# Kernel optimization log

Measured on AMD Instinct MI355X. Metric: run time of the kernel, lower is better.

## Reference

```python
import jax, jax.numpy as jnp
import numpy as np

DIM = 1024
NUM_HEADS = 16
HEAD_DIM = DIM // NUM_HEADS
SCALE = HEAD_DIM ** -0.5


def setup_inputs() -> dict:
    key = jax.random.key(0)
    k1, k2, k3 = jax.random.split(key, 3)
    B, N = 2, 2048
    x = jax.random.normal(k1, (B, N, DIM), dtype=jnp.float32)
    # qkv: Linear(dim, 3*dim, bias=False); proj: Linear(dim, dim) with bias
    w_qkv = jax.random.normal(k2, (3 * DIM, DIM), dtype=jnp.float32) * (DIM ** -0.5)
    w_proj = jax.random.normal(k3, (DIM, DIM), dtype=jnp.float32) * (DIM ** -0.5)
    b_proj = jnp.zeros((DIM,), dtype=jnp.float32)
    return {"x": x, "w_qkv": w_qkv, "w_proj": w_proj, "b_proj": b_proj}


def reference(x, w_qkv, w_proj, b_proj):
    B, N, C = x.shape
    H, D = NUM_HEADS, HEAD_DIM
    qkv = jnp.einsum('bnc,fc->bnf', x, w_qkv)                 # [B,N,3C]
    qkv = qkv.reshape(B, N, 3, H, D).transpose(2, 0, 3, 1, 4)  # [3,B,H,N,D]
    q, k, v = qkv[0], qkv[1], qkv[2]
    q = q * SCALE
    attn = jnp.einsum('bhnd,bhmd->bhnm', q, k)                 # [B,H,N,N]
    attn = jax.nn.softmax(attn, axis=-1)
    out = jnp.einsum('bhnm,bhmd->bhnd', attn, v)               # [B,H,N,D]
    out = out.transpose(0, 2, 1, 3).reshape(B, N, C)
    out = jnp.einsum('bnc,fc->bnf', out, w_proj) + b_proj
    return out
```

## Files before the change

### kernel.cpp

```cpp
#include <hip/hip_runtime.h>
#include <hip/hip_bf16.h>
#include <stdint.h>

typedef __attribute__((ext_vector_type(4))) float f32x4;
typedef __attribute__((ext_vector_type(16))) float f32x16;
typedef __attribute__((ext_vector_type(8))) short bf16x8;
typedef __attribute__((ext_vector_type(4))) short bf16x4;
typedef unsigned short ushort_t;

#define QSCALE 0.18033688f

__device__ inline short f2bf(float f) {
  unsigned u = __builtin_bit_cast(unsigned, f);
  u += 0x7fffu + ((u >> 16) & 1u);
  return (short)(u >> 16);
}

__device__ inline void gload_lds16(const void* g, void* l) {
  __builtin_amdgcn_global_load_lds(
      (const __attribute__((address_space(1))) void*)g,
      (__attribute__((address_space(3))) void*)l, 16, 0, 0);
}

__device__ inline unsigned cvtpk(float a, float b) {
  unsigned r;
  asm("v_cvt_pk_bf16_f32 %0, %1, %2" : "=v"(r) : "v"(a), "v"(b));
  return r;
}

__device__ inline void swap32u(unsigned& a, unsigned& b) {
  asm("v_permlane32_swap_b32 %0, %1" : "+v"(a), "+v"(b));
}

__global__ __launch_bounds__(256) void cvt_all(const float* __restrict__ x,
                                               const float* __restrict__ wq,
                                               const float* __restrict__ wp,
                                               short* __restrict__ Xb,
                                               short* __restrict__ Wq,
                                               short* __restrict__ Wp) {
  int i = blockIdx.x * 256 + threadIdx.x;
  const float* s;
  short* d;
  int off;
  if (i < 524288)       { s = x;  d = Xb; off = i; }
  else if (i < 917504)  { s = wq; d = Wq; off = i - 524288; }
  else                  { s = wp; d = Wp; off = i - 917504; }
  const float4* sv = (const float4*)s;
  float4 a = sv[2 * off], b = sv[2 * off + 1];
  bf16x8 o;
  o[0] = f2bf(a.x); o[1] = f2bf(a.y); o[2] = f2bf(a.z); o[3] = f2bf(a.w);
  o[4] = f2bf(b.x); o[5] = f2bf(b.y); o[6] = f2bf(b.z); o[7] = f2bf(b.w);
  ((bf16x8*)d)[off] = o;
}

template <int BN, int F32OUT>
__global__ __launch_bounds__(256, 3) void gemm_pipe(const short* __restrict__ A,
                                                    const short* __restrict__ B,
                                                    void* __restrict__ Cv,
                                                    const float* __restrict__ bias,
                                                    int scale_cols, float scale_val,
                                                    int M, int N, int K) {
  constexpr int MFR = (BN == 128) ? 4 : 2;
  __shared__ short Abuf[3][128 * 32];
  __shared__ short Bbuf[3][BN * 32];
  const int tid = threadIdx.x, wv = tid >> 6, ln = tid & 63;
  const int wm = (BN == 128) ? (wv >> 1) : wv;
  const int wn = (BN == 128) ? (wv & 1) : 0;
  const int bn0 = blockIdx.x * BN, bm0 = blockIdx.y * 128;
  const int nt = K >> 5;

  const int srow = ln >> 2;
  const int scol = (((ln & 3) ^ (srow & 3)) * 8);
  const int fln = ln & 15;
  const int fk = ln >> 4;

  f32x4 acc[MFR][4] = {};

  auto stage = [&](int t, int s) {
    const size_t k0 = (size_t)(t << 5);
#pragma unroll
    for (int rd = 0; rd < 2; rd++) {
      int ch = 2 * wv + rd;
      gload_lds16(A + (size_t)(bm0 + ch * 16 + srow) * K + k0 + scol,
                  (char*)Abuf[s] + ch * 1024);
    }
    if constexpr (BN == 128) {
#pragma unroll
      for (int rd = 0; rd < 2; rd++) {
        int ch = 2 * wv + rd;
        gload_lds16(B + (size_t)(bn0 + ch * 16 + srow) * K + k0 + scol,
                    (char*)Bbuf[s] + ch * 1024);
      }
    } else {
      gload_lds16(B + (size_t)(bn0 + wv * 16 + srow) * K + k0 + scol,
                  (char*)Bbuf[s] + wv * 1024);
    }
  };

  stage(0, 0);
  stage(1, 1);
  if constexpr (BN == 128) asm volatile("s_waitcnt vmcnt(4)" ::: "memory");
  else                     asm volatile("s_waitcnt vmcnt(3)" ::: "memory");
  __builtin_amdgcn_s_barrier();
  __builtin_amdgcn_sched_barrier(0);

  for (int t = 0; t < nt; t++) {
    const int s = t % 3;
    const bool more = (t + 2) < nt;
    if (more) stage(t + 2, (t + 2) % 3);

    const char* Ab = (const char*)Abuf[s];
    const char* Bb = (const char*)Bbuf[s];
    bf16x8 af[MFR], bfr[4];
#pragma unroll
    for (int m = 0; m < MFR; m++) {
      int R = wm * (MFR * 16) + m * 16 + fln;
      af[m] = *(const bf16x8*)(Ab + R * 64 + ((fk ^ (R & 3)) << 4));
    }
#pragma unroll
    for (int n = 0; n < 4; n++) {
      int R = wn * 64 + n * 16 + fln;
      bfr[n] = *(const bf16x8*)(Bb + R * 64 + ((fk ^ (R & 3)) << 4));
    }

    __builtin_amdgcn_s_setprio(1);
#pragma unroll
    for (int m = 0; m < MFR; m++)
#pragma unroll
      for (int n = 0; n < 4; n++)
        acc[m][n] = __builtin_amdgcn_mfma_f32_16x16x32_bf16(af[m], bfr[n], acc[m][n], 0, 0, 0);
    __builtin_amdgcn_s_setprio(0);

    if (more) {
      if constexpr (BN == 128) asm volatile("s_waitcnt vmcnt(4)" ::: "memory");
      else                     asm volatile("s_waitcnt vmcnt(3)" ::: "memory");
    } else {
      asm volatile("s_waitcnt vmcnt(0)" ::: "memory");
    }
    __builtin_amdgcn_s_barrier();
    __builtin_amdgcn_sched_barrier(0);
  }

  const int r0 = bm0 + wm * (MFR * 16), c0 = bn0 + wn * 64;
  const int fg4 = (ln >> 4) * 4;
#pragma unroll
  for (int m = 0; m < MFR; m++)
#pragma unroll
    for (int n = 0; n < 4; n++)
#pragma unroll
      for (int j = 0; j < 4; j++) {
        int row = r0 + m * 16 + fg4 + j;
        int col = c0 + n * 16 + fln;
        float v = acc[m][n][j];
        if (col < scale_cols) v *= scale_val;
        if (F32OUT) ((float*)Cv)[(size_t)row * N + col] = v + bias[col];
        else        ((short*)Cv)[(size_t)row * N + col] = f2bf(v);
      }
}

__global__ __launch_bounds__(256, 2) void attn_fwd(const short* __restrict__ QKV,
                                                   short* __restrict__ AO) {
  __shared__ short Ks[2][64 * 64];
  __shared__ short Vt[2][64 * 64];
  const int tid = threadIdx.x, wv = tid >> 6, ln = tid & 63;
  const int lq = ln & 31, hi = ln >> 5;
  const int id = blockIdx.x;
  const int c = (id & 7) * 64 + (id >> 3);
  const int qt = c & 15, bh = c >> 4;
  const int b = bh >> 4, h = bh & 15;
  const short* base = QKV + (size_t)b * 2048 * 3072 + h * 64;
  const short* Kg = base + 1024;
  const short* Vg = base + 2048;
  const int qrow = qt * 128 + wv * 32 + lq;

  bf16x8 qf[4];
  {
    const short* Qrow = base + (size_t)qrow * 3072;
#pragma unroll
    for (int ds = 0; ds < 4; ds++)
      qf[ds] = *(const bf16x8*)(Qrow + ds * 16 + hi * 8);
  }

  const int krow = ln >> 3;
  const int kcol = ((ln & 7) ^ (ln >> 3)) * 8;
  const int vrow_b = ln * 128;
  const int vxor = ln & 7;

  float l_run = 0.f;
  f32x16 o0 = {}, o1 = {};
  ushort_t vu[16];

#pragma unroll
  for (int rd = 0; rd < 2; rd++)
    gload_lds16(Kg + (size_t)(16 * wv + 8 * rd + krow) * 3072 + kcol,
                (char*)Ks[0] + (2 * wv + rd) * 1024);
#pragma unroll
  for (int i = 0; i < 16; i++)
    vu[i] = *(const ushort_t*)(Vg + (size_t)(16 * wv + i) * 3072 + ln);
  {
    bf16x8 w0, w1;
#pragma unroll
    for (int i = 0; i < 8; i++) { w0[i] = (short)vu[i]; w1[i] = (short)vu[8 + i]; }
    *(bf16x8*)((char*)Vt[0] + vrow_b + (((2 * wv) ^ vxor) << 4)) = w0;
    *(bf16x8*)((char*)Vt[0] + vrow_b + (((2 * wv + 1) ^ vxor) << 4)) = w1;
  }
  __syncthreads();

  for (int t = 0; t < 32; t++) {
    const int s = t & 1;
    if (t < 31) {
#pragma unroll
      for (int rd = 0; rd < 2; rd++)
        gload_lds16(Kg + (size_t)((t + 1) * 64 + 16 * wv + 8 * rd + krow) * 3072 + kcol,
                    (char*)Ks[s ^ 1] + (2 * wv + rd) * 1024);
#pragma unroll
      for (int i = 0; i < 16; i++)
        vu[i] = *(const ushort_t*)(Vg + (size_t)((t + 1) * 64 + 16 * wv + i) * 3072 + ln);
    }

    f32x16 c0 = {}, c1 = {};
    const char* Kb = (const char*)Ks[s];
    __builtin_amdgcn_s_setprio(1);
#pragma unroll
    for (int ds = 0; ds < 4; ds++) {
      const int cp = (ds * 2 + hi) ^ (lq & 7);
      bf16x8 ka0 = *(const bf16x8*)(Kb + lq * 128 + cp * 16);
      bf16x8 ka1 = *(const bf16x8*)(Kb + (32 + lq) * 128 + cp * 16);
      c0 = __builtin_amdgcn_mfma_f32_32x32x16_bf16(ka0, qf[ds], c0, 0, 0, 0);
      c1 = __builtin_amdgcn_mfma_f32_32x32x16_bf16(ka1, qf[ds], c1, 0, 0, 0);
    }
    __builtin_amdgcn_s_setprio(0);

#pragma unroll
    for (int r = 0; r < 16; r++) c0[r] = __builtin_amdgcn_exp2f(c0[r]);
#pragma unroll
    for (int r = 0; r < 16; r++) c1[r] = __builtin_amdgcn_exp2f(c1[r]);
    {
      float st[8];
#pragma unroll
      for (int r = 0; r < 8; r++)
        st[r] = (c0[2 * r] + c0[2 * r + 1]) + (c1[2 * r] + c1[2 * r + 1]);
#pragma unroll
      for (int r = 0; r < 4; r++) st[r] += st[r + 4];
      l_run += (st[0] + st[1]) + (st[2] + st[3]);
    }

    bf16x8 pa[4];
#pragma unroll
    for (int cs = 0; cs < 2; cs++) {
      const f32x16& p = cs ? c1 : c0;
#pragma unroll
      for (int ksl = 0; ksl < 2; ksl++) {
        unsigned A0 = cvtpk(p[8 * ksl + 0], p[8 * ksl + 1]);
        unsigned A1 = cvtpk(p[8 * ksl + 2], p[8 * ksl + 3]);
        unsigned B0 = cvtpk(p[8 * ksl + 4], p[8 * ksl + 5]);
        unsigned B1 = cvtpk(p[8 * ksl + 6], p[8 * ksl + 7]);
        swap32u(A0, B0);
        swap32u(A1, B1);
        union { unsigned u[4]; bf16x8 v; } tmp;
        tmp.u[0] = A0; tmp.u[1] = A1; tmp.u[2] = B0; tmp.u[3] = B1;
        pa[cs * 2 + ksl] = tmp.v;
      }
    }

    const char* Vb = (const char*)Vt[s];
    __builtin_amdgcn_s_setprio(1);
#pragma unroll
    for (int ks = 0; ks < 4; ks++) {
      const int cp = (ks * 2 + hi) ^ (lq & 7);
      bf16x8 va0 = *(const bf16x8*)(Vb + lq * 128 + cp * 16);
      bf16x8 va1 = *(const bf16x8*)(Vb + (32 + lq) * 128 + cp * 16);
      o0 = __builtin_amdgcn_mfma_f32_32x32x16_bf16(va0, pa[ks], o0, 0, 0, 0);
      o1 = __builtin_amdgcn_mfma_f32_32x32x16_bf16(va1, pa[ks], o1, 0, 0, 0);
    }
    __builtin_amdgcn_s_setprio(0);

    if (t < 31) {
      bf16x8 w0, w1;
#pragma unroll
      for (int i = 0; i < 8; i++) { w0[i] = (short)vu[i]; w1[i] = (short)vu[8 + i]; }
      *(bf16x8*)((char*)Vt[s ^ 1] + vrow_b + (((2 * wv) ^ vxor) << 4)) = w0;
      *(bf16x8*)((char*)Vt[s ^ 1] + vrow_b + (((2 * wv + 1) ^ vxor) << 4)) = w1;
    }
    __syncthreads();
  }

  l_run += __shfl_xor(l_run, 32);
  const float inv = __builtin_amdgcn_rcpf(l_run);
  short* Arow = AO + ((size_t)(b * 2048) + qrow) * 1024 + h * 64;
#pragma unroll
  for (int dt = 0; dt < 2; dt++) {
    const f32x16& o = dt ? o1 : o0;
#pragma unroll
    for (int g = 0; g < 4; g++) {
      bf16x4 w;
#pragma unroll
      for (int i = 0; i < 4; i++) w[i] = f2bf(o[4 * g + i] * inv);
      *(bf16x4*)(Arow + dt * 32 + 8 * g + 4 * hi) = w;
    }
  }
}

extern "C" void kernel_launch(void* const* d_in, const int* in_sizes, int n_in,
                              void* d_out, int out_size, void* d_ws, size_t ws_size,
                              hipStream_t stream) {
  const float* x = (const float*)d_in[0];
  const float* w_qkv = (const float*)d_in[1];
  const float* w_proj = (const float*)d_in[2];
  const float* b_proj = (const float*)d_in[3];
  float* out = (float*)d_out;

  char* ws = (char*)d_ws;
  short* Xb = (short*)(ws + 0);
  short* Wq = (short*)(ws + 8388608);
  short* Wp = (short*)(ws + 14680064);
  short* QKV = (short*)(ws + 16777216);
  short* AO = (short*)(ws + 41943040);

  cvt_all<<<4096, 256, 0, stream>>>(x, w_qkv, w_proj, Xb, Wq, Wp);

  gemm_pipe<128, 0><<<dim3(24, 32), 256, 0, stream>>>(Xb, Wq, QKV, nullptr,
                                                      1024, QSCALE, 4096, 3072, 1024);

  attn_fwd<<<dim3(512), 256, 0, stream>>>(QKV, AO);

  gemm_pipe<64, 1><<<dim3(16, 32), 256, 0, stream>>>(AO, Wp, out, b_proj,
                                                     0, 1.0f, 4096, 1024, 1024);
}
```

Before: 120.4 us.

## Double attention KV tile to 128 keys with split accumulators and earlier V store

```diff
diff --git a/kernel.cpp b/kernel.cpp
--- a/kernel.cpp
+++ b/kernel.cpp
@@ -160,8 +160,8 @@
 
 __global__ __launch_bounds__(256, 2) void attn_fwd(const short* __restrict__ QKV,
                                                    short* __restrict__ AO) {
-  __shared__ short Ks[2][64 * 64];
-  __shared__ short Vt[2][64 * 64];
+  __shared__ short Ks[2][128 * 64];
+  __shared__ short Vt[2][64 * 128];
   const int tid = threadIdx.x, wv = tid >> 6, ln = tid & 63;
   const int lq = ln & 31, hi = ln >> 5;
   const int id = blockIdx.x;
@@ -183,83 +183,116 @@
 
   const int krow = ln >> 3;
   const int kcol = ((ln & 7) ^ (ln >> 3)) * 8;
-  const int vrow_b = ln * 128;
-  const int vxor = ln & 7;
+  const int vrow_b = ln * 256;
+  const int vx = ln & 15;
 
   float l_run = 0.f;
-  f32x16 o0 = {}, o1 = {};
-  ushort_t vu[16];
-
-#pragma unroll
-  for (int rd = 0; rd < 2; rd++)
-    gload_lds16(Kg + (size_t)(16 * wv + 8 * rd + krow) * 3072 + kcol,
-                (char*)Ks[0] + (2 * wv + rd) * 1024);
-#pragma unroll
-  for (int i = 0; i < 16; i++)
-    vu[i] = *(const ushort_t*)(Vg + (size_t)(16 * wv + i) * 3072 + ln);
-  {
-    bf16x8 w0, w1;
-#pragma unroll
-    for (int i = 0; i < 8; i++) { w0[i] = (short)vu[i]; w1[i] = (short)vu[8 + i]; }
-    *(bf16x8*)((char*)Vt[0] + vrow_b + (((2 * wv) ^ vxor) << 4)) = w0;
-    *(bf16x8*)((char*)Vt[0] + vrow_b + (((2 * wv + 1) ^ vxor) << 4)) = w1;
-  }
+  f32x16 oA0 = {}, oA1 = {}, oB0 = {}, oB1 = {};
+  ushort_t vu[32];
+
+#define STAGE_K(ph, s)                                                           \
+  {                                                                              \
+    _Pragma("unroll")                                                            \
+    for (int rd = 0; rd < 4; rd++)                                               \
+      gload_lds16(Kg + (size_t)((ph) * 128 + 32 * wv + 8 * rd + krow) * 3072 + kcol, \
+                  (char*)Ks[s] + (4 * wv + rd) * 1024);                          \
+  }
+#define LOAD_V(ph)                                                               \
+  {                                                                              \
+    _Pragma("unroll")                                                            \
+    for (int i = 0; i < 32; i++)                                                 \
+      vu[i] = *(const ushort_t*)(Vg + (size_t)((ph) * 128 + 32 * wv + i) * 3072 + ln); \
+  }
+#define WRITE_V(s)                                                               \
+  {                                                                              \
+    _Pragma("unroll")                                                            \
+    for (int i = 0; i < 4; i++) {                                                \
+      bf16x8 w;                                                                  \
+      _Pragma("unroll")                                                          \
+      for (int j = 0; j < 8; j++) w[j] = (short)vu[8 * i + j];                   \
+      *(bf16x8*)((char*)Vt[s] + vrow_b + (((4 * wv + i) ^ vx) << 4)) = w;        \
+    }                                                                            \
+  }
+
+  STAGE_K(0, 0);
+  LOAD_V(0);
+  WRITE_V(0);
   __syncthreads();
 
-  for (int t = 0; t < 32; t++) {
+  for (int t = 0; t < 16; t++) {
     const int s = t & 1;
-    if (t < 31) {
-#pragma unroll
-      for (int rd = 0; rd < 2; rd++)
-        gload_lds16(Kg + (size_t)((t + 1) * 64 + 16 * wv + 8 * rd + krow) * 3072 + kcol,
-                    (char*)Ks[s ^ 1] + (2 * wv + rd) * 1024);
-#pragma unroll
-      for (int i = 0; i < 16; i++)
-        vu[i] = *(const ushort_t*)(Vg + (size_t)((t + 1) * 64 + 16 * wv + i) * 3072 + ln);
-    }
-
-    f32x16 c0 = {}, c1 = {};
+    if (t < 15) {
+      STAGE_K(t + 1, s ^ 1);
+      LOAD_V(t + 1);
+    }
+
+    f32x16 cA0 = {}, cA1 = {}, cB0 = {}, cB1 = {};
     const char* Kb = (const char*)Ks[s];
     __builtin_amdgcn_s_setprio(1);
 #pragma unroll
     for (int ds = 0; ds < 4; ds++) {
-      const int cp = (ds * 2 + hi) ^ (lq & 7);
-      bf16x8 ka0 = *(const bf16x8*)(Kb + lq * 128 + cp * 16);
-      bf16x8 ka1 = *(const bf16x8*)(Kb + (32 + lq) * 128 + cp * 16);
-      c0 = __builtin_amdgcn_mfma_f32_32x32x16_bf16(ka0, qf[ds], c0, 0, 0, 0);
-      c1 = __builtin_amdgcn_mfma_f32_32x32x16_bf16(ka1, qf[ds], c1, 0, 0, 0);
+      const int cp = ((ds * 2 + hi) ^ (lq & 7)) << 4;
+      bf16x8 kA0 = *(const bf16x8*)(Kb + lq * 128 + cp);
+      bf16x8 kA1 = *(const bf16x8*)(Kb + (32 + lq) * 128 + cp);
+      bf16x8 kB0 = *(const bf16x8*)(Kb + (64 + lq) * 128 + cp);
+      bf16x8 kB1 = *(const bf16x8*)(Kb + (96 + lq) * 128 + cp);
+      cA0 = __builtin_amdgcn_mfma_f32_32x32x16_bf16(kA0, qf[ds], cA0, 0, 0, 0);
+      cB0 = __builtin_amdgcn_mfma_f32_32x32x16_bf16(kB0, qf[ds], cB0, 0, 0, 0);
+      cA1 = __builtin_amdgcn_mfma_f32_32x32x16_bf16(kA1, qf[ds], cA1, 0, 0, 0);
+      cB1 = __builtin_amdgcn_mfma_f32_32x32x16_bf16(kB1, qf[ds], cB1, 0, 0, 0);
     }
     __builtin_amdgcn_s_setprio(0);
 
-#pragma unroll
-    for (int r = 0; r < 16; r++) c0[r] = __builtin_amdgcn_exp2f(c0[r]);
-#pragma unroll
-    for (int r = 0; r < 16; r++) c1[r] = __builtin_amdgcn_exp2f(c1[r]);
+    if (t < 15) WRITE_V(s ^ 1);
+
+#pragma unroll
+    for (int r = 0; r < 16; r++) cA0[r] = __builtin_amdgcn_exp2f(cA0[r]);
+#pragma unroll
+    for (int r = 0; r < 16; r++) cA1[r] = __builtin_amdgcn_exp2f(cA1[r]);
+#pragma unroll
+    for (int r = 0; r < 16; r++) cB0[r] = __builtin_amdgcn_exp2f(cB0[r]);
+#pragma unroll
+    for (int r = 0; r < 16; r++) cB1[r] = __builtin_amdgcn_exp2f(cB1[r]);
     {
       float st[8];
 #pragma unroll
       for (int r = 0; r < 8; r++)
-        st[r] = (c0[2 * r] + c0[2 * r + 1]) + (c1[2 * r] + c1[2 * r + 1]);
+        st[r] = ((cA0[2 * r] + cA0[2 * r + 1]) + (cA1[2 * r] + cA1[2 * r + 1])) +
+                ((cB0[2 * r] + cB0[2 * r + 1]) + (cB1[2 * r] + cB1[2 * r + 1]));
 #pragma unroll
       for (int r = 0; r < 4; r++) st[r] += st[r + 4];
       l_run += (st[0] + st[1]) + (st[2] + st[3]);
     }
 
-    bf16x8 pa[4];
+    bf16x8 paA[4], paB[4];
 #pragma unroll
     for (int cs = 0; cs < 2; cs++) {
-      const f32x16& p = cs ? c1 : c0;
+      const f32x16& pA = cs ? cA1 : cA0;
+      const f32x16& pB = cs ? cB1 : cB0;
 #pragma unroll
       for (int ksl = 0; ksl < 2; ksl++) {
-        unsigned A0 = cvtpk(p[8 * ksl + 0], p[8 * ksl + 1]);
-        unsigned A1 = cvtpk(p[8 * ksl + 2], p[8 * ksl + 3]);
-        unsigned B0 = cvtpk(p[8 * ksl + 4], p[8 * ksl + 5]);
-        unsigned B1 = cvtpk(p[8 * ksl + 6], p[8 * ksl + 7]);
-        swap32u(A0, B0);
-        swap32u(A1, B1);
-        union { unsigned u[4]; bf16x8 v; } tmp;
-        tmp.u[0] = A0; tmp.u[1] = A1; tmp.u[2] = B0; tmp.u[3] = B1;
-        pa[cs * 2 + ksl] = tmp.v;
+        {
+          unsigned A0 = cvtpk(pA[8 * ksl + 0], pA[8 * ksl + 1]);
+          unsigned A1 = cvtpk(pA[8 * ksl + 2], pA[8 * ksl + 3]);
+          unsigned B0 = cvtpk(pA[8 * ksl + 4], pA[8 * ksl + 5]);
+          unsigned B1 = cvtpk(pA[8 * ksl + 6], pA[8 * ksl + 7]);
+          swap32u(A0, B0);
+          swap32u(A1, B1);
+          union { unsigned u[4]; bf16x8 v; } tmp;
+          tmp.u[0] = A0; tmp.u[1] = A1; tmp.u[2] = B0; tmp.u[3] = B1;
+          paA[cs * 2 + ksl] = tmp.v;
+        }
+        {
+          unsigned A0 = cvtpk(pB[8 * ksl + 0], pB[8 * ksl + 1]);
+          unsigned A1 = cvtpk(pB[8 * ksl + 2], pB[8 * ksl + 3]);
+          unsigned B0 = cvtpk(pB[8 * ksl + 4], pB[8 * ksl + 5]);
+          unsigned B1 = cvtpk(pB[8 * ksl + 6], pB[8 * ksl + 7]);
+          swap32u(A0, B0);
+          swap32u(A1, B1);
+          union { unsigned u[4]; bf16x8 v; } tmp;
+          tmp.u[0] = A0; tmp.u[1] = A1; tmp.u[2] = B0; tmp.u[3] = B1;
+          paB[cs * 2 + ksl] = tmp.v;
+        }
       }
     }
 
@@ -267,35 +300,37 @@
     __builtin_amdgcn_s_setprio(1);
 #pragma unroll
     for (int ks = 0; ks < 4; ks++) {
-      const int cp = (ks * 2 + hi) ^ (lq & 7);
-      bf16x8 va0 = *(const bf16x8*)(Vb + lq * 128 + cp * 16);
-      bf16x8 va1 = *(const bf16x8*)(Vb + (32 + lq) * 128 + cp * 16);
-      o0 = __builtin_amdgcn_mfma_f32_32x32x16_bf16(va0, pa[ks], o0, 0, 0, 0);
-      o1 = __builtin_amdgcn_mfma_f32_32x32x16_bf16(va1, pa[ks], o1, 0, 0, 0);
+      const int cpa = (((ks * 2 + hi) ^ (lq & 15)) << 4);
+      const int cpb = (((8 + ks * 2 + hi) ^ (lq & 15)) << 4);
+      bf16x8 vA0 = *(const bf16x8*)(Vb + lq * 256 + cpa);
+      bf16x8 vA1 = *(const bf16x8*)(Vb + (32 + lq) * 256 + cpa);
+      bf16x8 vB0 = *(const bf16x8*)(Vb + lq * 256 + cpb);
+      bf16x8 vB1 = *(const bf16x8*)(Vb + (32 + lq) * 256 + cpb);
+      oA0 = __builtin_amdgcn_mfma_f32_32x32x16_bf16(vA0, paA[ks], oA0, 0, 0, 0);
+      oB0 = __builtin_amdgcn_mfma_f32_32x32x16_bf16(vB0, paB[ks], oB0, 0, 0, 0);
+      oA1 = __builtin_amdgcn_mfma_f32_32x32x16_bf16(vA1, paA[ks], oA1, 0, 0, 0);
+      oB1 = __builtin_amdgcn_mfma_f32_32x32x16_bf16(vB1, paB[ks], oB1, 0, 0, 0);
     }
     __builtin_amdgcn_s_setprio(0);
 
-    if (t < 31) {
-      bf16x8 w0, w1;
-#pragma unroll
-      for (int i = 0; i < 8; i++) { w0[i] = (short)vu[i]; w1[i] = (short)vu[8 + i]; }
-      *(bf16x8*)((char*)Vt[s ^ 1] + vrow_b + (((2 * wv) ^ vxor) << 4)) = w0;
-      *(bf16x8*)((char*)Vt[s ^ 1] + vrow_b + (((2 * wv + 1) ^ vxor) << 4)) = w1;
-    }
     __syncthreads();
   }
+#undef STAGE_K
+#undef LOAD_V
+#undef WRITE_V
 
   l_run += __shfl_xor(l_run, 32);
   const float inv = __builtin_amdgcn_rcpf(l_run);
   short* Arow = AO + ((size_t)(b * 2048) + qrow) * 1024 + h * 64;
 #pragma unroll
   for (int dt = 0; dt < 2; dt++) {
-    const f32x16& o = dt ? o1 : o0;
+    const f32x16& oa = dt ? oA1 : oA0;
+    const f32x16& ob = dt ? oB1 : oB0;
 #pragma unroll
     for (int g = 0; g < 4; g++) {
       bf16x4 w;
 #pragma unroll
-      for (int i = 0; i < 4; i++) w[i] = f2bf(o[4 * g + i] * inv);
+      for (int i = 0; i < 4; i++) w[i] = f2bf((oa[4 * g + i] + ob[4 * g + i]) * inv);
       *(bf16x4*)(Arow + dt * 32 + 8 * g + 4 * hi) = w;
     }
   }
```

Result: faster. 117.7 us (-2.2%).

## Split attention KV range in two with a separate merge kernel

Applied to the files above, without the earlier changes.

```diff
diff --git a/kernel.cpp b/kernel.cpp
--- a/kernel.cpp
+++ b/kernel.cpp
@@ -14,6 +14,10 @@
   unsigned u = __builtin_bit_cast(unsigned, f);
   u += 0x7fffu + ((u >> 16) & 1u);
   return (short)(u >> 16);
+}
+
+__device__ inline float bf2f(short s) {
+  return __builtin_bit_cast(float, ((unsigned)(ushort_t)s) << 16);
 }
 
 __device__ inline void gload_lds16(const void* g, void* l) {
@@ -158,19 +162,20 @@
       }
 }
 
-__global__ __launch_bounds__(256, 2) void attn_fwd(const short* __restrict__ QKV,
-                                                   short* __restrict__ AO) {
+__global__ __launch_bounds__(256, 4) void attn_fwd(const short* __restrict__ QKV,
+                                                   short* __restrict__ OP,
+                                                   float* __restrict__ Lp) {
   __shared__ short Ks[2][64 * 64];
   __shared__ short Vt[2][64 * 64];
   const int tid = threadIdx.x, wv = tid >> 6, ln = tid & 63;
   const int lq = ln & 31, hi = ln >> 5;
   const int id = blockIdx.x;
-  const int c = (id & 7) * 64 + (id >> 3);
-  const int qt = c & 15, bh = c >> 4;
+  const int c = (id & 7) * 128 + (id >> 3);
+  const int kvs = c & 1, qt = (c >> 1) & 15, bh = c >> 5;
   const int b = bh >> 4, h = bh & 15;
   const short* base = QKV + (size_t)b * 2048 * 3072 + h * 64;
-  const short* Kg = base + 1024;
-  const short* Vg = base + 2048;
+  const short* Kg = base + 1024 + (size_t)(kvs << 10) * 3072;
+  const short* Vg = base + 2048 + (size_t)(kvs << 10) * 3072;
   const int qrow = qt * 128 + wv * 32 + lq;
 
   bf16x8 qf[4];
@@ -206,9 +211,9 @@
   }
   __syncthreads();
 
-  for (int t = 0; t < 32; t++) {
+  for (int t = 0; t < 16; t++) {
     const int s = t & 1;
-    if (t < 31) {
+    if (t < 15) {
 #pragma unroll
       for (int rd = 0; rd < 2; rd++)
         gload_lds16(Kg + (size_t)((t + 1) * 64 + 16 * wv + 8 * rd + krow) * 3072 + kcol,
@@ -275,7 +280,7 @@
     }
     __builtin_amdgcn_s_setprio(0);
 
-    if (t < 31) {
+    if (t < 15) {
       bf16x8 w0, w1;
 #pragma unroll
       for (int i = 0; i < 8; i++) { w0[i] = (short)vu[i]; w1[i] = (short)vu[8 + i]; }
@@ -286,8 +291,9 @@
   }
 
   l_run += __shfl_xor(l_run, 32);
-  const float inv = __builtin_amdgcn_rcpf(l_run);
-  short* Arow = AO + ((size_t)(b * 2048) + qrow) * 1024 + h * 64;
+  const int qcol = wv * 32 + lq;
+  if (hi == 0) Lp[c * 128 + qcol] = l_run;
+  short* Op = OP + (size_t)c * 8192 + qcol * 64;
 #pragma unroll
   for (int dt = 0; dt < 2; dt++) {
     const f32x16& o = dt ? o1 : o0;
@@ -295,9 +301,35 @@
     for (int g = 0; g < 4; g++) {
       bf16x4 w;
 #pragma unroll
-      for (int i = 0; i < 4; i++) w[i] = f2bf(o[4 * g + i] * inv);
-      *(bf16x4*)(Arow + dt * 32 + 8 * g + 4 * hi) = w;
-    }
+      for (int i = 0; i < 4; i++) w[i] = f2bf(o[4 * g + i]);
+      *(bf16x4*)(Op + dt * 32 + 8 * g + 4 * hi) = w;
+    }
+  }
+}
+
+__global__ __launch_bounds__(256) void attn_merge(const short* __restrict__ OP,
+                                                  const float* __restrict__ Lp,
+                                                  short* __restrict__ AO) {
+  const int m = blockIdx.x;
+  const int bh = m >> 4, qt = m & 15;
+  const int b = bh >> 4, h = bh & 15;
+  const int tid = threadIdx.x;
+  const int q = tid & 127, dh = tid >> 7;
+  const int c0 = bh * 32 + qt * 2, c1 = c0 + 1;
+  const float l = Lp[c0 * 128 + q] + Lp[c1 * 128 + q];
+  const float inv = __builtin_amdgcn_rcpf(l);
+  const short* p0 = OP + (size_t)c0 * 8192 + q * 64 + dh * 32;
+  const short* p1 = OP + (size_t)c1 * 8192 + q * 64 + dh * 32;
+  short* dst = AO + ((size_t)(b * 2048 + qt * 128 + q)) * 1024 + h * 64 + dh * 32;
+#pragma unroll
+  for (int v = 0; v < 4; v++) {
+    bf16x8 a = ((const bf16x8*)p0)[v];
+    bf16x8 bb = ((const bf16x8*)p1)[v];
+    bf16x8 w;
+#pragma unroll
+    for (int j = 0; j < 8; j++)
+      w[j] = f2bf((bf2f(a[j]) + bf2f(bb[j])) * inv);
+    ((bf16x8*)dst)[v] = w;
   }
 }
 
@@ -316,13 +348,16 @@
   short* Wp = (short*)(ws + 14680064);
   short* QKV = (short*)(ws + 16777216);
   short* AO = (short*)(ws + 41943040);
+  float* Lp = (float*)(ws + 50331648);
+  short* OP = (short*)d_out;
 
   cvt_all<<<4096, 256, 0, stream>>>(x, w_qkv, w_proj, Xb, Wq, Wp);
 
   gemm_pipe<128, 0><<<dim3(24, 32), 256, 0, stream>>>(Xb, Wq, QKV, nullptr,
                                                       1024, QSCALE, 4096, 3072, 1024);
 
-  attn_fwd<<<dim3(512), 256, 0, stream>>>(QKV, AO);
+  attn_fwd<<<dim3(1024), 256, 0, stream>>>(QKV, OP, Lp);
+  attn_merge<<<dim3(512), 256, 0, stream>>>(OP, Lp, AO);
 
   gemm_pipe<64, 1><<<dim3(16, 32), 256, 0, stream>>>(AO, Wp, out, b_proj,
                                                      0, 1.0f, 4096, 1024, 1024);
```

New measurement: 127.7 us. +6.1%, slower.

## Write V transposed from QKV GEMM epilogue and stage it asynchronously in attention

Applied to the files above, without the earlier changes.

```diff
diff --git a/kernel.cpp b/kernel.cpp
--- a/kernel.cpp
+++ b/kernel.cpp
@@ -53,10 +53,11 @@
   ((bf16x8*)d)[off] = o;
 }
 
-template <int BN, int F32OUT>
+template <int BN, int F32OUT, int SPLITV>
 __global__ __launch_bounds__(256, 3) void gemm_pipe(const short* __restrict__ A,
                                                     const short* __restrict__ B,
                                                     void* __restrict__ Cv,
+                                                    short* __restrict__ Vtg,
                                                     const float* __restrict__ bias,
                                                     int scale_cols, float scale_val,
                                                     int M, int N, int K) {
@@ -144,21 +145,40 @@
   const int r0 = bm0 + wm * (MFR * 16), c0 = bn0 + wn * 64;
   const int fg4 = (ln >> 4) * 4;
 #pragma unroll
-  for (int m = 0; m < MFR; m++)
-#pragma unroll
-    for (int n = 0; n < 4; n++)
-#pragma unroll
-      for (int j = 0; j < 4; j++) {
-        int row = r0 + m * 16 + fg4 + j;
-        int col = c0 + n * 16 + fln;
-        float v = acc[m][n][j];
-        if (col < scale_cols) v *= scale_val;
-        if (F32OUT) ((float*)Cv)[(size_t)row * N + col] = v + bias[col];
-        else        ((short*)Cv)[(size_t)row * N + col] = f2bf(v);
+  for (int m = 0; m < MFR; m++) {
+    const int row0 = r0 + m * 16 + fg4;
+#pragma unroll
+    for (int n = 0; n < 4; n++) {
+      const int col = c0 + n * 16 + fln;
+      if constexpr (SPLITV) {
+        if (col < 2048) {
+          const float sc = (col < scale_cols) ? scale_val : 1.0f;
+#pragma unroll
+          for (int j = 0; j < 4; j++)
+            ((short*)Cv)[(size_t)(row0 + j) * 2048 + col] = f2bf(acc[m][n][j] * sc);
+        } else {
+          const int f = col - 2048, h = f >> 6, d = f & 63;
+          const int bb = row0 >> 11, ntok = row0 & 2047;
+          bf16x4 w;
+#pragma unroll
+          for (int j = 0; j < 4; j++) w[j] = f2bf(acc[m][n][j]);
+          *(bf16x4*)(Vtg + ((size_t)((bb * 16 + h) * 64 + d)) * 2048 + ntok) = w;
+        }
+      } else {
+#pragma unroll
+        for (int j = 0; j < 4; j++) {
+          float v = acc[m][n][j];
+          if (col < scale_cols) v *= scale_val;
+          if (F32OUT) ((float*)Cv)[(size_t)(row0 + j) * N + col] = v + bias[col];
+          else        ((short*)Cv)[(size_t)(row0 + j) * N + col] = f2bf(v);
+        }
       }
-}
-
-__global__ __launch_bounds__(256, 2) void attn_fwd(const short* __restrict__ QKV,
+    }
+  }
+}
+
+__global__ __launch_bounds__(256, 2) void attn_fwd(const short* __restrict__ QK,
+                                                   const short* __restrict__ Vtg,
                                                    short* __restrict__ AO) {
   __shared__ short Ks[2][64 * 64];
   __shared__ short Vt[2][64 * 64];
@@ -168,14 +188,14 @@
   const int c = (id & 7) * 64 + (id >> 3);
   const int qt = c & 15, bh = c >> 4;
   const int b = bh >> 4, h = bh & 15;
-  const short* base = QKV + (size_t)b * 2048 * 3072 + h * 64;
+  const short* base = QK + (size_t)(b * 2048) * 2048 + h * 64;
   const short* Kg = base + 1024;
-  const short* Vg = base + 2048;
+  const short* Vg = Vtg + (size_t)bh * 64 * 2048;
   const int qrow = qt * 128 + wv * 32 + lq;
 
   bf16x8 qf[4];
   {
-    const short* Qrow = base + (size_t)qrow * 3072;
+    const short* Qrow = base + (size_t)qrow * 2048;
 #pragma unroll
     for (int ds = 0; ds < 4; ds++)
       qf[ds] = *(const bf16x8*)(Qrow + ds * 16 + hi * 8);
@@ -183,40 +203,28 @@
 
   const int krow = ln >> 3;
   const int kcol = ((ln & 7) ^ (ln >> 3)) * 8;
-  const int vrow_b = ln * 128;
-  const int vxor = ln & 7;
 
   float l_run = 0.f;
   f32x16 o0 = {}, o1 = {};
-  ushort_t vu[16];
-
-#pragma unroll
-  for (int rd = 0; rd < 2; rd++)
-    gload_lds16(Kg + (size_t)(16 * wv + 8 * rd + krow) * 3072 + kcol,
-                (char*)Ks[0] + (2 * wv + rd) * 1024);
-#pragma unroll
-  for (int i = 0; i < 16; i++)
-    vu[i] = *(const ushort_t*)(Vg + (size_t)(16 * wv + i) * 3072 + ln);
-  {
-    bf16x8 w0, w1;
-#pragma unroll
-    for (int i = 0; i < 8; i++) { w0[i] = (short)vu[i]; w1[i] = (short)vu[8 + i]; }
-    *(bf16x8*)((char*)Vt[0] + vrow_b + (((2 * wv) ^ vxor) << 4)) = w0;
-    *(bf16x8*)((char*)Vt[0] + vrow_b + (((2 * wv + 1) ^ vxor) << 4)) = w1;
-  }
+
+#define STAGE(t, s)                                                              \
+  {                                                                              \
+    _Pragma("unroll")                                                            \
+    for (int rd = 0; rd < 2; rd++) {                                             \
+      const int r8 = 16 * wv + 8 * rd + krow;                                    \
+      gload_lds16(Kg + (size_t)((t) * 64 + r8) * 2048 + kcol,                    \
+                  (char*)Ks[s] + (2 * wv + rd) * 1024);                          \
+      gload_lds16(Vg + (size_t)r8 * 2048 + (t) * 64 + kcol,                      \
+                  (char*)Vt[s] + (2 * wv + rd) * 1024);                          \
+    }                                                                            \
+  }
+
+  STAGE(0, 0);
   __syncthreads();
 
   for (int t = 0; t < 32; t++) {
     const int s = t & 1;
-    if (t < 31) {
-#pragma unroll
-      for (int rd = 0; rd < 2; rd++)
-        gload_lds16(Kg + (size_t)((t + 1) * 64 + 16 * wv + 8 * rd + krow) * 3072 + kcol,
-                    (char*)Ks[s ^ 1] + (2 * wv + rd) * 1024);
-#pragma unroll
-      for (int i = 0; i < 16; i++)
-        vu[i] = *(const ushort_t*)(Vg + (size_t)((t + 1) * 64 + 16 * wv + i) * 3072 + ln);
-    }
+    if (t < 31) STAGE(t + 1, s ^ 1);
 
     f32x16 c0 = {}, c1 = {};
     const char* Kb = (const char*)Ks[s];
@@ -275,15 +283,9 @@
     }
     __builtin_amdgcn_s_setprio(0);
 
-    if (t < 31) {
-      bf16x8 w0, w1;
-#pragma unroll
-      for (int i = 0; i < 8; i++) { w0[i] = (short)vu[i]; w1[i] = (short)vu[8 + i]; }
-      *(bf16x8*)((char*)Vt[s ^ 1] + vrow_b + (((2 * wv) ^ vxor) << 4)) = w0;
-      *(bf16x8*)((char*)Vt[s ^ 1] + vrow_b + (((2 * wv + 1) ^ vxor) << 4)) = w1;
-    }
     __syncthreads();
   }
+#undef STAGE
 
   l_run += __shfl_xor(l_run, 32);
   const float inv = __builtin_amdgcn_rcpf(l_run);
@@ -311,19 +313,20 @@
   float* out = (float*)d_out;
 
   char* ws = (char*)d_ws;
-  short* Xb = (short*)(ws + 0);
-  short* Wq = (short*)(ws + 8388608);
-  short* Wp = (short*)(ws + 14680064);
-  short* QKV = (short*)(ws + 16777216);
-  short* AO = (short*)(ws + 41943040);
+  short* Xb  = (short*)(ws + 0);
+  short* Wq  = (short*)(ws + 8388608);
+  short* Wp  = (short*)(ws + 14680064);
+  short* QK  = (short*)(ws + 16777216);
+  short* Vtg = (short*)(ws + 33554432);
+  short* AO  = (short*)(ws + 41943040);
 
   cvt_all<<<4096, 256, 0, stream>>>(x, w_qkv, w_proj, Xb, Wq, Wp);
 
-  gemm_pipe<128, 0><<<dim3(24, 32), 256, 0, stream>>>(Xb, Wq, QKV, nullptr,
-                                                      1024, QSCALE, 4096, 3072, 1024);
-
-  attn_fwd<<<dim3(512), 256, 0, stream>>>(QKV, AO);
-
-  gemm_pipe<64, 1><<<dim3(16, 32), 256, 0, stream>>>(AO, Wp, out, b_proj,
-                                                     0, 1.0f, 4096, 1024, 1024);
-}
+  gemm_pipe<128, 0, 1><<<dim3(24, 32), 256, 0, stream>>>(Xb, Wq, QK, Vtg, nullptr,
+                                                         1024, QSCALE, 4096, 3072, 1024);
+
+  attn_fwd<<<dim3(512), 256, 0, stream>>>(QK, Vtg, AO);
+
+  gemm_pipe<64, 1, 0><<<dim3(16, 32), 256, 0, stream>>>(AO, Wp, out, nullptr, b_proj,
+                                                        0, 1.0f, 4096, 1024, 1024);
+}
```

New measurement: 114.4 us. -5.0%, faster.
